# Optimization experiments

Measured on AMD Instinct MI355X. Metric: run time of the kernel, lower is better.

Reference implementation:

```python
import jax, jax.numpy as jnp
import numpy as np

B, S, D, H = 4, 2048, 512, 8
HD = D // H


def _xavier(key, shape):
    fan_in, fan_out = shape[1], shape[0]
    limit = float(np.sqrt(6.0 / (fan_in + fan_out)))
    return jax.random.uniform(key, shape, jnp.float32, -limit, limit)


def setup_inputs() -> dict:
    key = jax.random.key(0)
    ks = jax.random.split(key, 7)
    return {
        "query": jax.random.normal(ks[0], (B, S, D), jnp.float32),
        "key": jax.random.normal(ks[1], (B, S, D), jnp.float32),
        "value": jax.random.normal(ks[2], (B, S, D), jnp.float32),
        "Wq": _xavier(ks[3], (D, D)), "bq": jnp.zeros((D,), jnp.float32),
        "Wk": _xavier(ks[4], (D, D)), "bk": jnp.zeros((D,), jnp.float32),
        "Wv": _xavier(ks[5], (D, D)), "bv": jnp.zeros((D,), jnp.float32),
        "Wo": _xavier(ks[6], (D, D)), "bo": jnp.zeros((D,), jnp.float32),
    }


def _split_heads(x):
    # [B,S,D] -> [B,H,S,HD]
    return x.reshape(B, S, H, HD).transpose(0, 2, 1, 3)


def reference(query, key, value, Wq, bq, Wk, bk, Wv, bv, Wo, bo):
    # torch Linear: y = x @ W.T + b
    Q = _split_heads(query @ Wq.T + bq)
    K = _split_heads(key @ Wk.T + bk)
    V = _split_heads(value @ Wv.T + bv)
    scale = 1.0 / jnp.sqrt(jnp.asarray(HD, Q.dtype))
    logits = jnp.einsum("bhqd,bhkd->bhqk", Q, K) * scale  # [B,H,S,S]
    attn = jax.nn.softmax(logits, axis=-1)
    ctx = jnp.einsum("bhqk,bhkd->bhqd", attn, V)
    ctx = ctx.transpose(0, 2, 1, 3).reshape(B, S, D)
    return ctx @ Wo.T + bo
```

## Files before the change

kernel.cpp:

```cpp
#include <hip/hip_runtime.h>
#include <hip/hip_bf16.h>


#define BB 4
#define SS 2048
#define DD 512
#define HH 8
#define HDD 64

typedef __bf16 bf16;
typedef __bf16 bf16x8 __attribute__((ext_vector_type(8)));
typedef float f32x4 __attribute__((ext_vector_type(4)));

__device__ __forceinline__ int swz(int row, int byteInRow) {
    return row * 128 + (byteInRow ^ ((row & 7) << 4));
}

__device__ __forceinline__ void gload16(const void* g, void* l) {
    __builtin_amdgcn_global_load_lds(
        (const __attribute__((address_space(1))) void*)g,
        (__attribute__((address_space(3))) void*)l, 16, 0, 0);
}

__global__ __launch_bounds__(256) void gemm_qkv(
    const float* __restrict__ Xq, const float* __restrict__ Xk, const float* __restrict__ Xv,
    const float* __restrict__ Wq, const float* __restrict__ Wk, const float* __restrict__ Wv,
    const float* __restrict__ bq, const float* __restrict__ bk, const float* __restrict__ bv,
    bf16* __restrict__ Qb, bf16* __restrict__ Kb, bf16* __restrict__ Vt)
{
    const int z = blockIdx.z;
    const float* __restrict__ A    = (z == 0) ? Xq : (z == 1) ? Xk : Xv;
    const float* __restrict__ W    = (z == 0) ? Wq : (z == 1) ? Wk : Wv;
    const float* __restrict__ bias = (z == 0) ? bq : (z == 1) ? bk : bv;

    __shared__ char lds[32768];
    char* As = lds;
    char* Bs = lds + 16384;

    const int t = threadIdx.x, wid = t >> 6, lane = t & 63;
    const int m0 = blockIdx.y * 128, n0 = blockIdx.x * 128;
    const int wr = wid >> 1, wc = wid & 1;
    const int lr = lane & 15, lg = lane >> 4;

    float bv4[4];
#pragma unroll
    for (int ni = 0; ni < 4; ni++) bv4[ni] = bias[n0 + wc * 64 + ni * 16 + lr];

    f32x4 acc[4][4] = {};

    for (int k0 = 0; k0 < DD; k0 += 64) {
#pragma unroll
        for (int i = 0; i < 8; i++) {
            int g = t + i * 256;
            int row = g >> 4, c4 = g & 15;
            float4 va = *(const float4*)&A[(size_t)(m0 + row) * DD + k0 + c4 * 4];
            float4 vb = *(const float4*)&W[(size_t)(n0 + row) * DD + k0 + c4 * 4];
            union { bf16 h[4]; ushort4 u; } ca, cb;
            ca.h[0] = (bf16)va.x; ca.h[1] = (bf16)va.y; ca.h[2] = (bf16)va.z; ca.h[3] = (bf16)va.w;
            cb.h[0] = (bf16)vb.x; cb.h[1] = (bf16)vb.y; cb.h[2] = (bf16)vb.z; cb.h[3] = (bf16)vb.w;
            *(ushort4*)(As + swz(row, c4 * 8)) = ca.u;
            *(ushort4*)(Bs + swz(row, c4 * 8)) = cb.u;
        }
        __syncthreads();
#pragma unroll
        for (int kk = 0; kk < 2; kk++) {
            bf16x8 af[4], bfr[4];
#pragma unroll
            for (int mi = 0; mi < 4; mi++)
                af[mi] = *(const bf16x8*)(As + swz(wr * 64 + mi * 16 + lr, kk * 64 + lg * 16));
#pragma unroll
            for (int ni = 0; ni < 4; ni++)
                bfr[ni] = *(const bf16x8*)(Bs + swz(wc * 64 + ni * 16 + lr, kk * 64 + lg * 16));
#pragma unroll
            for (int mi = 0; mi < 4; mi++)
#pragma unroll
                for (int ni = 0; ni < 4; ni++)
                    acc[mi][ni] = __builtin_amdgcn_mfma_f32_16x16x32_bf16(af[mi], bfr[ni], acc[mi][ni], 0, 0, 0);
        }
        __syncthreads();
    }

#pragma unroll
    for (int mi = 0; mi < 4; mi++)
#pragma unroll
        for (int ni = 0; ni < 4; ni++) {
            int col = n0 + wc * 64 + ni * 16 + lr;
#pragma unroll
            for (int j = 0; j < 4; j++) {
                int row = m0 + wr * 64 + mi * 16 + lg * 4 + j;
                float v = acc[mi][ni][j] + bv4[ni];
                if (z == 0) {
                    Qb[(size_t)row * DD + col] = (bf16)v;
                } else if (z == 1) {
                    Kb[(size_t)row * DD + col] = (bf16)v;
                } else {
                    int b = row >> 11, s = row & 2047, h = col >> 6, d = col & 63;
                    Vt[((((size_t)b * HH + h) * HDD + d) << 11) + s] = (bf16)v;
                }
            }
        }
}

__global__ __launch_bounds__(512) void attn_kernel(
    const bf16* __restrict__ Qb, const bf16* __restrict__ Kb,
    const bf16* __restrict__ Vt, bf16* __restrict__ Ctx)
{
    __shared__ char lds[49152];
    const int t = threadIdx.x, wid = t >> 6, lane = t & 63;
    const int lr = lane & 15, lg = lane >> 4;
    const int b = blockIdx.y >> 3, h = blockIdx.y & 7;
    const int q0 = blockIdx.x * 128 + wid * 16;

    const bf16* Qp = Qb + ((size_t)b * SS + q0) * DD + h * HDD;
    const bf16* Kp = Kb + (size_t)b * SS * DD + h * HDD;
    const bf16* Vp = Vt + ((size_t)b * HH + h) * HDD * SS;

    const float qscale = 0.125f * 1.4426950408889634f;
    bf16x8 qf[2];
#pragma unroll
    for (int kk = 0; kk < 2; kk++) {
        bf16x8 v = *(const bf16x8*)(Qp + (size_t)lr * DD + kk * 32 + lg * 8);
#pragma unroll
        for (int e = 0; e < 8; e++) v[e] = (bf16)((float)v[e] * qscale);
        qf[kk] = v;
    }

    bf16x8 ones;
#pragma unroll
    for (int e = 0; e < 8; e++) ones[e] = (bf16)1.0f;

    const int srow = lane >> 3;
    const int s_l  = (lane & 7) ^ srow;
    const int r0 = 8 * wid + srow;
    const size_t koff = (size_t)r0 * DD + s_l * 8;
    const size_t voff = (size_t)r0 * SS + s_l * 8;

#define STAGE(buf, kvb) do {                                                   \
        char* Kd = lds + (buf) * 8192 + wid * 1024;                            \
        char* Vd = lds + 16384 + (buf) * 8192 + wid * 1024;                    \
        gload16(Kp + koff + (size_t)(kvb) * DD, Kd);                           \
        gload16(Vp + voff + (kvb), Vd);                                        \
    } while (0)

    STAGE(0, 0);

    f32x4 ctx[4] = {};
    f32x4 l4 = {};

    __syncthreads();

    const int NT = SS / 64;
    for (int it = 0; it < NT; ++it) {
        const int cur = it & 1;
        const char* Ks = lds + cur * 8192;
        const char* Vs = lds + 16384 + cur * 8192;
        char* Ps = lds + 32768 + wid * 2048;

        if (it + 1 < NT) STAGE(cur ^ 1, (it + 1) * 64);

        f32x4 sc[4];
#pragma unroll
        for (int nt = 0; nt < 4; nt++) {
            bf16x8 kf0 = *(const bf16x8*)(Ks + swz(nt * 16 + lr, lg * 16));
            bf16x8 kf1 = *(const bf16x8*)(Ks + swz(nt * 16 + lr, 64 + lg * 16));
            f32x4 a = {};
            a = __builtin_amdgcn_mfma_f32_16x16x32_bf16(qf[0], kf0, a, 0, 0, 0);
            a = __builtin_amdgcn_mfma_f32_16x16x32_bf16(qf[1], kf1, a, 0, 0, 0);
            sc[nt] = a;
        }

#pragma unroll
        for (int nt = 0; nt < 4; nt++)
#pragma unroll
            for (int j = 0; j < 4; j++)
                sc[nt][j] = __builtin_amdgcn_exp2f(sc[nt][j]);

#pragma unroll
        for (int nt = 0; nt < 4; nt++)
#pragma unroll
            for (int j = 0; j < 4; j++)
                *(bf16*)(Ps + swz(lg * 4 + j, (nt * 16 + lr) * 2)) = (bf16)sc[nt][j];

        bf16x8 pf0 = *(const bf16x8*)(Ps + swz(lr, lg * 16));
        bf16x8 pf1 = *(const bf16x8*)(Ps + swz(lr, 64 + lg * 16));

        l4 = __builtin_amdgcn_mfma_f32_16x16x32_bf16(pf0, ones, l4, 0, 0, 0);
        l4 = __builtin_amdgcn_mfma_f32_16x16x32_bf16(pf1, ones, l4, 0, 0, 0);

#pragma unroll
        for (int dt = 0; dt < 4; dt++) {
            bf16x8 vf0 = *(const bf16x8*)(Vs + swz(dt * 16 + lr, lg * 16));
            bf16x8 vf1 = *(const bf16x8*)(Vs + swz(dt * 16 + lr, 64 + lg * 16));
            ctx[dt] = __builtin_amdgcn_mfma_f32_16x16x32_bf16(pf0, vf0, ctx[dt], 0, 0, 0);
            ctx[dt] = __builtin_amdgcn_mfma_f32_16x16x32_bf16(pf1, vf1, ctx[dt], 0, 0, 0);
        }
        __syncthreads();
    }

#undef STAGE

#pragma unroll
    for (int dt = 0; dt < 4; dt++)
#pragma unroll
        for (int j = 0; j < 4; j++) {
            int qrow = q0 + lg * 4 + j;
            int col = h * HDD + dt * 16 + lr;
            Ctx[((size_t)b * SS + qrow) * DD + col] = (bf16)(ctx[dt][j] / l4[j]);
        }
}

__global__ __launch_bounds__(256) void gemm_out(
    const bf16* __restrict__ A, const float* __restrict__ W,
    const float* __restrict__ bias, float* __restrict__ Out)
{
    __shared__ char lds[32768];
    char* As = lds;
    char* Bs = lds + 16384;

    const int t = threadIdx.x, wid = t >> 6, lane = t & 63;
    const int m0 = blockIdx.y * 128, n0 = blockIdx.x * 128;
    const int wr = wid >> 1, wc = wid & 1;
    const int lr = lane & 15, lg = lane >> 4;

    float bv4[4];
#pragma unroll
    for (int ni = 0; ni < 4; ni++) bv4[ni] = bias[n0 + wc * 64 + ni * 16 + lr];

    f32x4 acc[4][4] = {};

    for (int k0 = 0; k0 < DD; k0 += 64) {
#pragma unroll
        for (int i = 0; i < 4; i++) {
            int g = t + i * 256;
            int row = g >> 3, sl = g & 7;
            *(uint4*)(As + swz(row, sl * 16)) = *(const uint4*)&A[(size_t)(m0 + row) * DD + k0 + sl * 8];
        }
#pragma unroll
        for (int i = 0; i < 8; i++) {
            int g = t + i * 256;
            int row = g >> 4, c4 = g & 15;
            float4 vb = *(const float4*)&W[(size_t)(n0 + row) * DD + k0 + c4 * 4];
            union { bf16 h[4]; ushort4 u; } cb;
            cb.h[0] = (bf16)vb.x; cb.h[1] = (bf16)vb.y; cb.h[2] = (bf16)vb.z; cb.h[3] = (bf16)vb.w;
            *(ushort4*)(Bs + swz(row, c4 * 8)) = cb.u;
        }
        __syncthreads();
#pragma unroll
        for (int kk = 0; kk < 2; kk++) {
            bf16x8 af[4], bfr[4];
#pragma unroll
            for (int mi = 0; mi < 4; mi++)
                af[mi] = *(const bf16x8*)(As + swz(wr * 64 + mi * 16 + lr, kk * 64 + lg * 16));
#pragma unroll
            for (int ni = 0; ni < 4; ni++)
                bfr[ni] = *(const bf16x8*)(Bs + swz(wc * 64 + ni * 16 + lr, kk * 64 + lg * 16));
#pragma unroll
            for (int mi = 0; mi < 4; mi++)
#pragma unroll
                for (int ni = 0; ni < 4; ni++)
                    acc[mi][ni] = __builtin_amdgcn_mfma_f32_16x16x32_bf16(af[mi], bfr[ni], acc[mi][ni], 0, 0, 0);
        }
        __syncthreads();
    }

#pragma unroll
    for (int mi = 0; mi < 4; mi++)
#pragma unroll
        for (int ni = 0; ni < 4; ni++) {
            int col = n0 + wc * 64 + ni * 16 + lr;
#pragma unroll
            for (int j = 0; j < 4; j++) {
                int row = m0 + wr * 64 + mi * 16 + lg * 4 + j;
                Out[(size_t)row * DD + col] = acc[mi][ni][j] + bv4[ni];
            }
        }
}

extern "C" void kernel_launch(void* const* d_in, const int* in_sizes, int n_in,
                              void* d_out, int out_size, void* d_ws, size_t ws_size,
                              hipStream_t stream) {
    (void)in_sizes; (void)n_in; (void)out_size; (void)ws_size;
    const float* q  = (const float*)d_in[0];
    const float* k  = (const float*)d_in[1];
    const float* v  = (const float*)d_in[2];
    const float* Wq = (const float*)d_in[3]; const float* bq = (const float*)d_in[4];
    const float* Wk = (const float*)d_in[5]; const float* bk = (const float*)d_in[6];
    const float* Wv = (const float*)d_in[7]; const float* bv = (const float*)d_in[8];
    const float* Wo = (const float*)d_in[9]; const float* bo = (const float*)d_in[10];
    float* out = (float*)d_out;

    char* ws = (char*)d_ws;
    const size_t MD2 = (size_t)BB * SS * DD * 2;
    bf16* Qb  = (bf16*)(ws);
    bf16* Kb  = (bf16*)(ws + MD2);
    bf16* Vt  = (bf16*)(ws + 2 * MD2);
    bf16* Ctx = (bf16*)(ws + 3 * MD2);

    dim3 gQKV(DD / 128, (BB * SS) / 128, 3);
    gemm_qkv<<<gQKV, 256, 0, stream>>>(q, k, v, Wq, Wk, Wv, bq, bk, bv, Qb, Kb, Vt);

    dim3 gA(SS / 128, BB * HH);
    attn_kernel<<<gA, 512, 0, stream>>>(Qb, Kb, Vt, Ctx);

    dim3 gO(DD / 128, (BB * SS) / 128);
    gemm_out<<<gO, 256, 0, stream>>>(Ctx, Wo, bo, out);
}
```

Baseline: 119.6 us.

## Pre-convert inputs to bf16 and use direct global-to-LDS loads with XCD-aware block remap

Adds a separate conversion kernel that casts the activations and all weights to bf16 in the workspace. Both GEMMs then stage tiles with global_load_lds 16-byte transfers into the swizzled LDS layout, replacing the register round-trip and in-loop conversion. The grids of all three kernels are flattened and remapped so consecutive blocks spread across the 8 XCDs. The cost is an extra kernel launch plus one full read and write pass over the fp32 inputs. The Ctx buffer is reused to hold the bf16 query copy before attention overwrites it.

```diff
diff --git a/kernel.cpp b/kernel.cpp
--- a/kernel.cpp
+++ b/kernel.cpp
@@ -22,15 +22,48 @@
         (__attribute__((address_space(3))) void*)l, 16, 0, 0);
 }
 
+__global__ __launch_bounds__(256) void cvt_bf16(
+    const float* __restrict__ xq, const float* __restrict__ xk, const float* __restrict__ xv,
+    const float* __restrict__ wq, const float* __restrict__ wk, const float* __restrict__ wv,
+    const float* __restrict__ wo,
+    bf16* __restrict__ xqb, bf16* __restrict__ xkb, bf16* __restrict__ xvb,
+    bf16* __restrict__ wqb, bf16* __restrict__ wkb, bf16* __restrict__ wvb,
+    bf16* __restrict__ wob)
+{
+    const int NX = BB * SS * DD / 4;
+    const int NW = DD * DD / 4;
+    const int total = 3 * NX + 4 * NW;
+    for (int g = blockIdx.x * 256 + threadIdx.x; g < total; g += gridDim.x * 256) {
+        const float* src; bf16* dst; int off;
+        if (g < 3 * NX) {
+            int s = g >> 20; off = g & (NX - 1);
+            src = s == 0 ? xq : s == 1 ? xk : xv;
+            dst = s == 0 ? xqb : s == 1 ? xkb : xvb;
+        } else {
+            int gg = g - 3 * NX; int s = gg >> 16; off = gg & (NW - 1);
+            src = s == 0 ? wq : s == 1 ? wk : s == 2 ? wv : wo;
+            dst = s == 0 ? wqb : s == 1 ? wkb : s == 2 ? wvb : wob;
+        }
+        float4 v = ((const float4*)src)[off];
+        union { bf16 h[4]; ushort4 u; } c;
+        c.h[0] = (bf16)v.x; c.h[1] = (bf16)v.y; c.h[2] = (bf16)v.z; c.h[3] = (bf16)v.w;
+        ((ushort4*)dst)[off] = c.u;
+    }
+}
+
 __global__ __launch_bounds__(256) void gemm_qkv(
-    const float* __restrict__ Xq, const float* __restrict__ Xk, const float* __restrict__ Xv,
-    const float* __restrict__ Wq, const float* __restrict__ Wk, const float* __restrict__ Wv,
+    const bf16* __restrict__ Xq, const bf16* __restrict__ Xk, const bf16* __restrict__ Xv,
+    const bf16* __restrict__ Wq, const bf16* __restrict__ Wk, const bf16* __restrict__ Wv,
     const float* __restrict__ bq, const float* __restrict__ bk, const float* __restrict__ bv,
     bf16* __restrict__ Qb, bf16* __restrict__ Kb, bf16* __restrict__ Vt)
 {
-    const int z = blockIdx.z;
-    const float* __restrict__ A    = (z == 0) ? Xq : (z == 1) ? Xk : Xv;
-    const float* __restrict__ W    = (z == 0) ? Wq : (z == 1) ? Wk : Wv;
+    const int lin = blockIdx.x;
+    const int w = (lin & 7) * 96 + (lin >> 3);
+    const int z = w >> 8, rem = w & 255;
+    const int m0 = (rem >> 2) * 128, n0 = (rem & 3) * 128;
+
+    const bf16* __restrict__ A  = (z == 0) ? Xq : (z == 1) ? Xk : Xv;
+    const bf16* __restrict__ Wt = (z == 0) ? Wq : (z == 1) ? Wk : Wv;
     const float* __restrict__ bias = (z == 0) ? bq : (z == 1) ? bk : bv;
 
     __shared__ char lds[32768];
@@ -38,7 +71,6 @@
     char* Bs = lds + 16384;
 
     const int t = threadIdx.x, wid = t >> 6, lane = t & 63;
-    const int m0 = blockIdx.y * 128, n0 = blockIdx.x * 128;
     const int wr = wid >> 1, wc = wid & 1;
     const int lr = lane & 15, lg = lane >> 4;
 
@@ -46,20 +78,17 @@
 #pragma unroll
     for (int ni = 0; ni < 4; ni++) bv4[ni] = bias[n0 + wc * 64 + ni * 16 + lr];
 
+    const int srow = lane >> 3;
+    const int s_l  = (lane & 7) ^ srow;
+
     f32x4 acc[4][4] = {};
 
     for (int k0 = 0; k0 < DD; k0 += 64) {
 #pragma unroll
-        for (int i = 0; i < 8; i++) {
-            int g = t + i * 256;
-            int row = g >> 4, c4 = g & 15;
-            float4 va = *(const float4*)&A[(size_t)(m0 + row) * DD + k0 + c4 * 4];
-            float4 vb = *(const float4*)&W[(size_t)(n0 + row) * DD + k0 + c4 * 4];
-            union { bf16 h[4]; ushort4 u; } ca, cb;
-            ca.h[0] = (bf16)va.x; ca.h[1] = (bf16)va.y; ca.h[2] = (bf16)va.z; ca.h[3] = (bf16)va.w;
-            cb.h[0] = (bf16)vb.x; cb.h[1] = (bf16)vb.y; cb.h[2] = (bf16)vb.z; cb.h[3] = (bf16)vb.w;
-            *(ushort4*)(As + swz(row, c4 * 8)) = ca.u;
-            *(ushort4*)(Bs + swz(row, c4 * 8)) = cb.u;
+        for (int i = 0; i < 4; i++) {
+            int row = 32 * wid + 8 * i + srow;
+            gload16(A  + (size_t)(m0 + row) * DD + k0 + s_l * 8, As + (32 * wid + 8 * i) * 128);
+            gload16(Wt + (size_t)(n0 + row) * DD + k0 + s_l * 8, Bs + (32 * wid + 8 * i) * 128);
         }
         __syncthreads();
 #pragma unroll
@@ -108,8 +137,11 @@
     __shared__ char lds[49152];
     const int t = threadIdx.x, wid = t >> 6, lane = t & 63;
     const int lr = lane & 15, lg = lane >> 4;
-    const int b = blockIdx.y >> 3, h = blockIdx.y & 7;
-    const int q0 = blockIdx.x * 128 + wid * 16;
+    const int lin = blockIdx.x;
+    const int wk_ = (lin & 7) * 64 + (lin >> 3);
+    const int qt = wk_ & 15, bh = wk_ >> 4;
+    const int b = bh >> 3, h = bh & 7;
+    const int q0 = qt * 128 + wid * 16;
 
     const bf16* Qp = Qb + ((size_t)b * SS + q0) * DD + h * HDD;
     const bf16* Kp = Kb + (size_t)b * SS * DD + h * HDD;
@@ -210,15 +242,18 @@
 }
 
 __global__ __launch_bounds__(256) void gemm_out(
-    const bf16* __restrict__ A, const float* __restrict__ W,
+    const bf16* __restrict__ A, const bf16* __restrict__ Wt,
     const float* __restrict__ bias, float* __restrict__ Out)
 {
+    const int lin = blockIdx.x;
+    const int w = (lin & 7) * 32 + (lin >> 3);
+    const int m0 = (w >> 2) * 128, n0 = (w & 3) * 128;
+
     __shared__ char lds[32768];
     char* As = lds;
     char* Bs = lds + 16384;
 
     const int t = threadIdx.x, wid = t >> 6, lane = t & 63;
-    const int m0 = blockIdx.y * 128, n0 = blockIdx.x * 128;
     const int wr = wid >> 1, wc = wid & 1;
     const int lr = lane & 15, lg = lane >> 4;
 
@@ -226,23 +261,17 @@
 #pragma unroll
     for (int ni = 0; ni < 4; ni++) bv4[ni] = bias[n0 + wc * 64 + ni * 16 + lr];
 
+    const int srow = lane >> 3;
+    const int s_l  = (lane & 7) ^ srow;
+
     f32x4 acc[4][4] = {};
 
     for (int k0 = 0; k0 < DD; k0 += 64) {
 #pragma unroll
         for (int i = 0; i < 4; i++) {
-            int g = t + i * 256;
-            int row = g >> 3, sl = g & 7;
-            *(uint4*)(As + swz(row, sl * 16)) = *(const uint4*)&A[(size_t)(m0 + row) * DD + k0 + sl * 8];
-        }
-#pragma unroll
-        for (int i = 0; i < 8; i++) {
-            int g = t + i * 256;
-            int row = g >> 4, c4 = g & 15;
-            float4 vb = *(const float4*)&W[(size_t)(n0 + row) * DD + k0 + c4 * 4];
-            union { bf16 h[4]; ushort4 u; } cb;
-            cb.h[0] = (bf16)vb.x; cb.h[1] = (bf16)vb.y; cb.h[2] = (bf16)vb.z; cb.h[3] = (bf16)vb.w;
-            *(ushort4*)(Bs + swz(row, c4 * 8)) = cb.u;
+            int row = 32 * wid + 8 * i + srow;
+            gload16(A  + (size_t)(m0 + row) * DD + k0 + s_l * 8, As + (32 * wid + 8 * i) * 128);
+            gload16(Wt + (size_t)(n0 + row) * DD + k0 + s_l * 8, Bs + (32 * wid + 8 * i) * 128);
         }
         __syncthreads();
 #pragma unroll
@@ -291,17 +320,26 @@
 
     char* ws = (char*)d_ws;
     const size_t MD2 = (size_t)BB * SS * DD * 2;
+    const size_t WB  = (size_t)DD * DD * 2;
     bf16* Qb  = (bf16*)(ws);
     bf16* Kb  = (bf16*)(ws + MD2);
     bf16* Vt  = (bf16*)(ws + 2 * MD2);
     bf16* Ctx = (bf16*)(ws + 3 * MD2);
-
-    dim3 gQKV(DD / 128, (BB * SS) / 128, 3);
-    gemm_qkv<<<gQKV, 256, 0, stream>>>(q, k, v, Wq, Wk, Wv, bq, bk, bv, Qb, Kb, Vt);
-
-    dim3 gA(SS / 128, BB * HH);
-    attn_kernel<<<gA, 512, 0, stream>>>(Qb, Kb, Vt, Ctx);
-
-    dim3 gO(DD / 128, (BB * SS) / 128);
-    gemm_out<<<gO, 256, 0, stream>>>(Ctx, Wo, bo, out);
-}
+    bf16* Xqb = Ctx;
+    bf16* Xkb = (bf16*)(ws + 4 * MD2);
+    bf16* Xvb = (bf16*)(ws + 5 * MD2);
+    bf16* Wqb = (bf16*)(ws + 6 * MD2);
+    bf16* Wkb = (bf16*)(ws + 6 * MD2 + WB);
+    bf16* Wvb = (bf16*)(ws + 6 * MD2 + 2 * WB);
+    bf16* Wob = (bf16*)(ws + 6 * MD2 + 3 * WB);
+
+    cvt_bf16<<<2048, 256, 0, stream>>>(q, k, v, Wq, Wk, Wv, Wo,
+                                       Xqb, Xkb, Xvb, Wqb, Wkb, Wvb, Wob);
+
+    gemm_qkv<<<768, 256, 0, stream>>>(Xqb, Xkb, Xvb, Wqb, Wkb, Wvb,
+                                      bq, bk, bv, Qb, Kb, Vt);
+
+    attn_kernel<<<512, 512, 0, stream>>>(Qb, Kb, Vt, Ctx);
+
+    gemm_out<<<256, 256, 0, stream>>>(Ctx, Wob, bo, out);
+}
```

Result: slower. 123.3 us (+3.1%).
